# Kernel optimization log

Measured on AMD Instinct MI355X. Metric: run time of the kernel, lower is better.

The kernel has to match this reference:

```python
import jax, jax.numpy as jnp
import numpy as np

N = 40000      # nodes
E = 640000     # edges (avg degree 16)
F_IN = 33      # input residue features (hard-coded in module)
H = 128        # hidden_channels
C_OUT = 3      # output classes (hard-coded)
L = 8          # num_layers
ALPHA = 0.1
THETA = 0.5


def setup_inputs() -> dict:
    key = jax.random.key(0)
    ks = jax.random.split(key, 8)
    x = jax.random.normal(ks[0], (N, F_IN), jnp.float32)
    edge_row = jax.random.randint(ks[1], (E,), 0, N)
    edge_col = jax.random.randint(ks[2], (E,), 0, N)
    edge_weight = jax.random.uniform(ks[3], (E,), jnp.float32)
    # nn.Linear stores weight as [out, in]
    W_in = jax.random.normal(ks[4], (H, F_IN), jnp.float32) * 0.1
    b_in = jnp.zeros((H,), jnp.float32)
    W_out = jax.random.normal(ks[5], (C_OUT, H), jnp.float32) * 0.1
    b_out = jnp.zeros((C_OUT,), jnp.float32)
    # GCN2Conv shared weight1 per layer: [L, H, H]
    W_conv = jax.random.normal(ks[6], (L, H, H), jnp.float32) * (1.0 / np.sqrt(H))
    return dict(x=x, edge_row=edge_row, edge_col=edge_col, edge_weight=edge_weight,
                W_in=W_in, b_in=b_in, W_out=W_out, b_out=b_out, W_conv=W_conv)


def reference(x, edge_row, edge_col, edge_weight, W_in, b_in, W_out, b_out, W_conv):
    # dropout p=0.0 -> identity (also eval mode)
    x0 = jax.nn.relu(x @ W_in.T + b_in)                      # [N, H]
    # GCN2Conv beta_l = log(theta / layer + 1), layer = 1..L
    betas = jnp.log(THETA / jnp.arange(1.0, L + 1.0, dtype=jnp.float32) + 1.0)

    def spmm(h):
        # adj_t @ h : gather source-node features, weight, scatter-add to rows
        return jax.ops.segment_sum(edge_weight[:, None] * h[edge_col], edge_row,
                                   num_segments=N)

    def step(xc, lw):
        W, beta = lw
        # GCN2Conv (shared_weights=True, normalize=False):
        #   xx = (1-alpha)*A@h + alpha*x0 ; out = (1-beta)*xx + beta*(xx@W)
        xx = (1.0 - ALPHA) * spmm(xc) + ALPHA * x0
        out = (1.0 - beta) * xx + beta * (xx @ W)
        return xc + jax.nn.relu(out), None                   # residual in GCN.forward

    x_final, _ = jax.lax.scan(step, x0, (W_conv, betas))
    return x_final @ W_out.T + b_out                          # [N, 3]
```

## Files before the change

### kernel.cpp

```cpp
#include <hip/hip_runtime.h>
#include <hip/hip_bf16.h>
#include <math.h>

#define N_NODES 40000
#define NE      640000
#define FIN     33
#define H       128
#define COUT    3
#define NLAYERS 8
#define ALPHA   0.1f
#define THETA   0.5f
#define CAP     96

typedef __bf16 bf16x8 __attribute__((ext_vector_type(8)));
typedef float  f32x4  __attribute__((ext_vector_type(4)));

__device__ inline unsigned short f2bf(float f) {
    __hip_bfloat16 b = __float2bfloat16(f);
    return *(unsigned short*)&b;
}
__device__ inline float bf2f(unsigned short u) {
    __hip_bfloat16 b = *(__hip_bfloat16*)&u;
    return __bfloat162float(b);
}

__global__ __launch_bounds__(256) void k_scatter(const int* __restrict__ row,
                          const int* __restrict__ col, const float* __restrict__ w,
                          int* __restrict__ cnt, unsigned int* __restrict__ bucket) {
    int e0 = (blockIdx.x * 256 + threadIdx.x) * 4;
    int r[4], pos[4];
    unsigned int rec[4];
    #pragma unroll
    for (int i = 0; i < 4; i++) {
        int e = e0 + i;
        r[i] = row[e];
        unsigned int wb = f2bf((1.0f - ALPHA) * w[e]);
        rec[i] = (wb << 16) | (unsigned int)col[e];
    }
    #pragma unroll
    for (int i = 0; i < 4; i++) pos[i] = atomicAdd(&cnt[r[i]], 1);
    #pragma unroll
    for (int i = 0; i < 4; i++) bucket[(size_t)r[i] * CAP + pos[i]] = rec[i];
}

__global__ __launch_bounds__(256) void k_wprep(const float* __restrict__ W,
                        unsigned short* __restrict__ Wtbf) {
    int idx = blockIdx.x * 256 + threadIdx.x;
    int l = idx >> 14;
    int rem = idx & 16383;
    int k = rem >> 7, j = rem & 127;
    Wtbf[l * 16384 + j * 128 + k] = f2bf(W[idx]);
}

__global__ __launch_bounds__(256) void k_xin(const float* __restrict__ x,
                      const float* __restrict__ Win, const float* __restrict__ bin,
                      unsigned short* __restrict__ x0bf,
                      unsigned short* __restrict__ hbf) {
    __shared__ float sW[H * FIN];
    __shared__ float sx[16][FIN];
    int t = threadIdx.x;
    for (int i = t; i < H * FIN; i += 256) sW[i] = Win[i];
    int n0 = blockIdx.x * 16;
    for (int i = t; i < 16 * FIN; i += 256)
        sx[i / FIN][i % FIN] = x[(size_t)(n0 + i / FIN) * FIN + (i % FIN)];
    __syncthreads();
    int f = t % H;
    int l0 = t / H;
    float bv = bin[f];
    for (int lo = l0; lo < 16; lo += 2) {
        float acc = bv;
        #pragma unroll
        for (int k = 0; k < FIN; k++) acc += sx[lo][k] * sW[f * FIN + k];
        acc = fmaxf(acc, 0.f);
        size_t idx = (size_t)(n0 + lo) * H + f;
        unsigned short b = f2bf(acc);
        x0bf[idx] = b;
        hbf[idx] = b;
    }
}

__global__ __launch_bounds__(256) void k_spmm(const int* __restrict__ cnt,
                       const unsigned int* __restrict__ bucket,
                       const unsigned short* __restrict__ hbf,
                       const unsigned short* __restrict__ x0bf,
                       unsigned short* __restrict__ xxbf) {
    int wave = (blockIdx.x * blockDim.x + threadIdx.x) >> 6;
    int lane = threadIdx.x & 63;
    if (wave >= N_NODES) return;
    int deg = cnt[wave];
    const unsigned int* ep = bucket + (size_t)wave * CAP;
    int slot = lane >> 4;
    int fid  = lane & 15;

    float acc[8] = {0,0,0,0,0,0,0,0};

    for (int e = 0; e < deg; e += 16) {
        unsigned int u[4];
        uint4 q[4];
        #pragma unroll
        for (int k = 0; k < 4; k++) {
            int ei = e + k * 4 + slot;
            unsigned int uu = ep[ei];
            u[k] = (ei < deg) ? uu : 0u;
        }
        #pragma unroll
        for (int k = 0; k < 4; k++)
            q[k] = *(const uint4*)(hbf + (size_t)(u[k] & 0xffffu) * H + fid * 8);
        #pragma unroll
        for (int k = 0; k < 4; k++) {
            float w = bf2f((unsigned short)(u[k] >> 16));
            acc[0] += w * bf2f((unsigned short)(q[k].x & 0xffffu));
            acc[1] += w * bf2f((unsigned short)(q[k].x >> 16));
            acc[2] += w * bf2f((unsigned short)(q[k].y & 0xffffu));
            acc[3] += w * bf2f((unsigned short)(q[k].y >> 16));
            acc[4] += w * bf2f((unsigned short)(q[k].z & 0xffffu));
            acc[5] += w * bf2f((unsigned short)(q[k].z >> 16));
            acc[6] += w * bf2f((unsigned short)(q[k].w & 0xffffu));
            acc[7] += w * bf2f((unsigned short)(q[k].w >> 16));
        }
    }

    #pragma unroll
    for (int j = 0; j < 8; j++) {
        acc[j] += __shfl_xor(acc[j], 16);
        acc[j] += __shfl_xor(acc[j], 32);
    }

    if (slot == 0) {
        uint4 xq = *(const uint4*)(x0bf + (size_t)wave * H + fid * 8);
        float o0 = acc[0] + ALPHA * bf2f((unsigned short)(xq.x & 0xffffu));
        float o1 = acc[1] + ALPHA * bf2f((unsigned short)(xq.x >> 16));
        float o2 = acc[2] + ALPHA * bf2f((unsigned short)(xq.y & 0xffffu));
        float o3 = acc[3] + ALPHA * bf2f((unsigned short)(xq.y >> 16));
        float o4 = acc[4] + ALPHA * bf2f((unsigned short)(xq.z & 0xffffu));
        float o5 = acc[5] + ALPHA * bf2f((unsigned short)(xq.z >> 16));
        float o6 = acc[6] + ALPHA * bf2f((unsigned short)(xq.w & 0xffffu));
        float o7 = acc[7] + ALPHA * bf2f((unsigned short)(xq.w >> 16));
        uint4 r;
        r.x = (unsigned int)f2bf(o0) | ((unsigned int)f2bf(o1) << 16);
        r.y = (unsigned int)f2bf(o2) | ((unsigned int)f2bf(o3) << 16);
        r.z = (unsigned int)f2bf(o4) | ((unsigned int)f2bf(o5) << 16);
        r.w = (unsigned int)f2bf(o6) | ((unsigned int)f2bf(o7) << 16);
        *(uint4*)(xxbf + (size_t)wave * H + fid * 8) = r;
    }
}

__global__ __launch_bounds__(128) void k_gemm(const unsigned short* __restrict__ xxbf,
                       const unsigned short* __restrict__ Wtbf,
                       unsigned short* __restrict__ hbf, float beta,
                       const float* __restrict__ Wout, const float* __restrict__ bout,
                       float* __restrict__ out, int do_out) {
    int t = threadIdx.x;
    int wv = t >> 6, lane = t & 63;
    int quad = lane >> 4, l16 = lane & 15;
    int rbase = blockIdx.x * 32 + wv * 16;

    f32x4 acc[8];
    #pragma unroll
    for (int j = 0; j < 8; j++) acc[j] = (f32x4){0.f, 0.f, 0.f, 0.f};

    #pragma unroll
    for (int k0 = 0; k0 < 4; k0++) {
        bf16x8 av = *(const bf16x8*)(xxbf + (size_t)(rbase + l16) * H + k0 * 32 + quad * 8);
        #pragma unroll
        for (int j = 0; j < 8; j++) {
            bf16x8 bv = *(const bf16x8*)(Wtbf + (size_t)(j * 16 + l16) * H + k0 * 32 + quad * 8);
            acc[j] = __builtin_amdgcn_mfma_f32_16x16x32_bf16(av, bv, acc[j], 0, 0, 0);
        }
    }

    float omb = 1.f - beta;
    float po[4][3];
    #pragma unroll
    for (int r = 0; r < 4; r++) { po[r][0] = 0.f; po[r][1] = 0.f; po[r][2] = 0.f; }

    #pragma unroll
    for (int j = 0; j < 8; j++) {
        int col = j * 16 + l16;
        float w0 = 0.f, w1 = 0.f, w2 = 0.f;
        if (do_out) { w0 = Wout[col]; w1 = Wout[H + col]; w2 = Wout[2 * H + col]; }
        #pragma unroll
        for (int r = 0; r < 4; r++) {
            int row = rbase + quad * 4 + r;
            size_t idx = (size_t)row * H + col;
            float sk = bf2f(xxbf[idx]);
            float o = omb * sk + beta * acc[j][r];
            float hv = bf2f(hbf[idx]) + fmaxf(o, 0.f);
            hbf[idx] = f2bf(hv);
            po[r][0] += hv * w0; po[r][1] += hv * w1; po[r][2] += hv * w2;
        }
    }

    if (do_out) {
        #pragma unroll
        for (int off = 1; off < 16; off <<= 1) {
            #pragma unroll
            for (int r = 0; r < 4; r++) {
                po[r][0] += __shfl_xor(po[r][0], off);
                po[r][1] += __shfl_xor(po[r][1], off);
                po[r][2] += __shfl_xor(po[r][2], off);
            }
        }
        if (l16 == 0) {
            #pragma unroll
            for (int r = 0; r < 4; r++) {
                int row = rbase + quad * 4 + r;
                out[(size_t)row * 3 + 0] = po[r][0] + bout[0];
                out[(size_t)row * 3 + 1] = po[r][1] + bout[1];
                out[(size_t)row * 3 + 2] = po[r][2] + bout[2];
            }
        }
    }
}

extern "C" void kernel_launch(void* const* d_in, const int* in_sizes, int n_in,
                              void* d_out, int out_size, void* d_ws, size_t ws_size,
                              hipStream_t stream) {
    const float* x     = (const float*)d_in[0];
    const int*   erow  = (const int*)  d_in[1];
    const int*   ecol  = (const int*)  d_in[2];
    const float* ew    = (const float*)d_in[3];
    const float* Win   = (const float*)d_in[4];
    const float* bin   = (const float*)d_in[5];
    const float* Wout  = (const float*)d_in[6];
    const float* bout  = (const float*)d_in[7];
    const float* Wconv = (const float*)d_in[8];
    float* out = (float*)d_out;

    char* ws = (char*)d_ws;
    const size_t NHb = (size_t)N_NODES * H * sizeof(unsigned short);
    unsigned short* xxbf  = (unsigned short*)(ws);
    unsigned short* x0bf  = (unsigned short*)(ws + NHb);
    unsigned short* hbf   = (unsigned short*)(ws + 2 * NHb);
    char* p = ws + 3 * NHb;
    unsigned short* Wtbf  = (unsigned short*)p;  p += 8 * H * H * 2;
    int*  cnt     = (int*) p;  p += 160256;
    unsigned int* bucket = (unsigned int*)p;

    hipMemsetAsync(cnt, 0, (size_t)N_NODES * 4, stream);
    k_scatter<<<NE / 1024, 256, 0, stream>>>(erow, ecol, ew, cnt, bucket);

    k_wprep<<<8 * H * H / 256, 256, 0, stream>>>(Wconv, Wtbf);
    k_xin  <<<N_NODES / 16,    256, 0, stream>>>(x, Win, bin, x0bf, hbf);

    for (int l = 0; l < NLAYERS; l++) {
        float beta = logf(THETA / (float)(l + 1) + 1.0f);
        k_spmm<<<N_NODES / 4,  256, 0, stream>>>(cnt, bucket, hbf, x0bf, xxbf);
        k_gemm<<<N_NODES / 32, 128, 0, stream>>>(xxbf, Wtbf + (size_t)l * H * H,
                                                 hbf, beta, Wout, bout, out,
                                                 (l == NLAYERS - 1) ? 1 : 0);
    }
}
```

Baseline: 469.8 us.

## Fold beta skip term into weights and merge setup kernels into one launch

The per-layer weight matrix becomes beta*W + (1-beta)*I at preparation time, so the GEMM epilogue no longer reloads xx or computes the blend. The scatter, weight-prep and input-projection kernels are combined into a single launch that picks its role from the block index. This removes one bf16 global load per output element in every layer and two launch gaps. The cost is that the identity term is now added after bf16 rounding inside the MFMA, which slightly changes numerics.

```diff
diff --git a/kernel.cpp b/kernel.cpp
--- a/kernel.cpp
+++ b/kernel.cpp
@@ -12,6 +12,10 @@
 #define THETA   0.5f
 #define CAP     96
 
+#define SB_SCAT 625
+#define SB_WPRE 512
+#define SB_XIN  2500
+
 typedef __bf16 bf16x8 __attribute__((ext_vector_type(8)));
 typedef float  f32x4  __attribute__((ext_vector_type(4)));
 
@@ -24,58 +28,65 @@
     return __bfloat162float(b);
 }
 
-__global__ __launch_bounds__(256) void k_scatter(const int* __restrict__ row,
-                          const int* __restrict__ col, const float* __restrict__ w,
-                          int* __restrict__ cnt, unsigned int* __restrict__ bucket) {
-    int e0 = (blockIdx.x * 256 + threadIdx.x) * 4;
-    int r[4], pos[4];
-    unsigned int rec[4];
-    #pragma unroll
-    for (int i = 0; i < 4; i++) {
-        int e = e0 + i;
-        r[i] = row[e];
-        unsigned int wb = f2bf((1.0f - ALPHA) * w[e]);
-        rec[i] = (wb << 16) | (unsigned int)col[e];
-    }
-    #pragma unroll
-    for (int i = 0; i < 4; i++) pos[i] = atomicAdd(&cnt[r[i]], 1);
-    #pragma unroll
-    for (int i = 0; i < 4; i++) bucket[(size_t)r[i] * CAP + pos[i]] = rec[i];
-}
-
-__global__ __launch_bounds__(256) void k_wprep(const float* __restrict__ W,
-                        unsigned short* __restrict__ Wtbf) {
-    int idx = blockIdx.x * 256 + threadIdx.x;
-    int l = idx >> 14;
-    int rem = idx & 16383;
-    int k = rem >> 7, j = rem & 127;
-    Wtbf[l * 16384 + j * 128 + k] = f2bf(W[idx]);
-}
-
-__global__ __launch_bounds__(256) void k_xin(const float* __restrict__ x,
-                      const float* __restrict__ Win, const float* __restrict__ bin,
-                      unsigned short* __restrict__ x0bf,
-                      unsigned short* __restrict__ hbf) {
+__global__ __launch_bounds__(256) void k_setup(
+        const int* __restrict__ row, const int* __restrict__ col,
+        const float* __restrict__ w, int* __restrict__ cnt,
+        unsigned int* __restrict__ bucket,
+        const float* __restrict__ Wconv, unsigned short* __restrict__ Wtbf,
+        const float* __restrict__ x, const float* __restrict__ Win,
+        const float* __restrict__ bin,
+        unsigned short* __restrict__ x0bf, unsigned short* __restrict__ hbf) {
     __shared__ float sW[H * FIN];
     __shared__ float sx[16][FIN];
-    int t = threadIdx.x;
-    for (int i = t; i < H * FIN; i += 256) sW[i] = Win[i];
-    int n0 = blockIdx.x * 16;
-    for (int i = t; i < 16 * FIN; i += 256)
-        sx[i / FIN][i % FIN] = x[(size_t)(n0 + i / FIN) * FIN + (i % FIN)];
-    __syncthreads();
-    int f = t % H;
-    int l0 = t / H;
-    float bv = bin[f];
-    for (int lo = l0; lo < 16; lo += 2) {
-        float acc = bv;
-        #pragma unroll
-        for (int k = 0; k < FIN; k++) acc += sx[lo][k] * sW[f * FIN + k];
-        acc = fmaxf(acc, 0.f);
-        size_t idx = (size_t)(n0 + lo) * H + f;
-        unsigned short b = f2bf(acc);
-        x0bf[idx] = b;
-        hbf[idx] = b;
+    int b = blockIdx.x, t = threadIdx.x;
+
+    if (b < SB_SCAT) {
+        int e0 = (b * 256 + t) * 4;
+        int r[4], pos[4];
+        unsigned int rec[4];
+        #pragma unroll
+        for (int i = 0; i < 4; i++) {
+            int e = e0 + i;
+            r[i] = row[e];
+            unsigned int wb = f2bf((1.0f - ALPHA) * w[e]);
+            rec[i] = (wb << 16) | (unsigned int)col[e];
+        }
+        #pragma unroll
+        for (int i = 0; i < 4; i++) pos[i] = atomicAdd(&cnt[r[i]], 1);
+        #pragma unroll
+        for (int i = 0; i < 4; i++) bucket[(size_t)r[i] * CAP + pos[i]] = rec[i];
+        return;
+    }
+    if (b < SB_SCAT + SB_WPRE) {
+        int idx = (b - SB_SCAT) * 256 + t;
+        int l = idx >> 14;
+        int rem = idx & 16383;
+        int k = rem >> 7, j = rem & 127;
+        float beta = logf(THETA / (float)(l + 1) + 1.0f);
+        float v = beta * Wconv[idx];
+        if (j == k) v += 1.0f - beta;
+        Wtbf[l * 16384 + j * 128 + k] = f2bf(v);
+        return;
+    }
+    {
+        int n0 = (b - SB_SCAT - SB_WPRE) * 16;
+        for (int i = t; i < H * FIN; i += 256) sW[i] = Win[i];
+        for (int i = t; i < 16 * FIN; i += 256)
+            sx[i / FIN][i % FIN] = x[(size_t)(n0 + i / FIN) * FIN + (i % FIN)];
+        __syncthreads();
+        int f = t % H;
+        int l0 = t / H;
+        float bv = bin[f];
+        for (int lo = l0; lo < 16; lo += 2) {
+            float acc = bv;
+            #pragma unroll
+            for (int k = 0; k < FIN; k++) acc += sx[lo][k] * sW[f * FIN + k];
+            acc = fmaxf(acc, 0.f);
+            size_t idx = (size_t)(n0 + lo) * H + f;
+            unsigned short bb = f2bf(acc);
+            x0bf[idx] = bb;
+            hbf[idx] = bb;
+        }
     }
 }
 
@@ -147,7 +158,7 @@
 
 __global__ __launch_bounds__(128) void k_gemm(const unsigned short* __restrict__ xxbf,
                        const unsigned short* __restrict__ Wtbf,
-                       unsigned short* __restrict__ hbf, float beta,
+                       unsigned short* __restrict__ hbf,
                        const float* __restrict__ Wout, const float* __restrict__ bout,
                        float* __restrict__ out, int do_out) {
     int t = threadIdx.x;
@@ -169,7 +180,6 @@
         }
     }
 
-    float omb = 1.f - beta;
     float po[4][3];
     #pragma unroll
     for (int r = 0; r < 4; r++) { po[r][0] = 0.f; po[r][1] = 0.f; po[r][2] = 0.f; }
@@ -183,9 +193,7 @@
         for (int r = 0; r < 4; r++) {
             int row = rbase + quad * 4 + r;
             size_t idx = (size_t)row * H + col;
-            float sk = bf2f(xxbf[idx]);
-            float o = omb * sk + beta * acc[j][r];
-            float hv = bf2f(hbf[idx]) + fmaxf(o, 0.f);
+            float hv = bf2f(hbf[idx]) + fmaxf(acc[j][r], 0.f);
             hbf[idx] = f2bf(hv);
             po[r][0] += hv * w0; po[r][1] += hv * w1; po[r][2] += hv * w2;
         }
@@ -238,16 +246,13 @@
     unsigned int* bucket = (unsigned int*)p;
 
     hipMemsetAsync(cnt, 0, (size_t)N_NODES * 4, stream);
-    k_scatter<<<NE / 1024, 256, 0, stream>>>(erow, ecol, ew, cnt, bucket);
-
-    k_wprep<<<8 * H * H / 256, 256, 0, stream>>>(Wconv, Wtbf);
-    k_xin  <<<N_NODES / 16,    256, 0, stream>>>(x, Win, bin, x0bf, hbf);
+    k_setup<<<SB_SCAT + SB_WPRE + SB_XIN, 256, 0, stream>>>(
+        erow, ecol, ew, cnt, bucket, Wconv, Wtbf, x, Win, bin, x0bf, hbf);
 
     for (int l = 0; l < NLAYERS; l++) {
-        float beta = logf(THETA / (float)(l + 1) + 1.0f);
         k_spmm<<<N_NODES / 4,  256, 0, stream>>>(cnt, bucket, hbf, x0bf, xxbf);
         k_gemm<<<N_NODES / 32, 128, 0, stream>>>(xxbf, Wtbf + (size_t)l * H * H,
-                                                 hbf, beta, Wout, bout, out,
+                                                 hbf, Wout, bout, out,
                                                  (l == NLAYERS - 1) ? 1 : 0);
     }
 }
```

New measurement: 459.3 us (median of 2 runs). 2.2% less time.
